# Kernel tuning notes

Measured on AMD Instinct MI355X. Metric: run time of the kernel, lower is better.

## Reference

```python
import jax, jax.numpy as jnp
import numpy as np

M1, M2 = 16, 16  # Fourier modes per dim


def conv1x1(x, w, b):
    # x: [B,Ci,H,W], w: [Co,Ci], b: [Co]
    return jnp.einsum('bihw,oi->bohw', x, w) + b[None, :, None, None]


def fno_block(x, wr, wi, bw, bb):
    # x: [B,C,H,W]; wr/wi: [C,C,M1,M2]; bw: [C,C]; bb: [C]
    H, W = x.shape[-2], x.shape[-1]
    x_fft = jnp.fft.rfftn(x, axes=(-2, -1), norm='ortho')[:, :, :M1, :M2]
    w = (wr + 1j * wi).astype(jnp.complex64)
    out_fft = jnp.einsum('bikl,iokl->bokl', x_fft, w)
    # irfftn with s zero-pads truncated modes back to full spatial size
    x_spec = jnp.fft.irfftn(out_fft, s=(H, W), axes=(-2, -1), norm='ortho')
    return jax.nn.gelu(x_spec + conv1x1(x, bw, bb), approximate=False)


def setup_inputs() -> dict:
    key = jax.random.key(0)
    ks = jax.random.split(key, 8)
    B, in_c, H, W = 4, 3, 256, 256
    out_c, n_blocks, width = 4, 4, 32
    scale = 1.0 / (width * width)
    return {
        'x': jax.random.normal(ks[0], (B, in_c, H, W), jnp.float32),
        'lift_w': jax.random.normal(ks[1], (width, in_c), jnp.float32) * 0.1,
        'lift_b': jnp.zeros((width,), jnp.float32),
        'wr': jax.random.normal(ks[2], (out_c, n_blocks, width, width, M1, M2), jnp.float32) * scale,
        'wi': jax.random.normal(ks[3], (out_c, n_blocks, width, width, M1, M2), jnp.float32) * scale,
        'byp_w': jax.random.normal(ks[4], (out_c, n_blocks, width, width), jnp.float32) * 0.1,
        'byp_b': jnp.zeros((out_c, n_blocks, width), jnp.float32),
        'proj_w': jax.random.normal(ks[5], (1, width), jnp.float32) * 0.1,
        'proj_b': jnp.zeros((1,), jnp.float32),
    }


def reference(x, lift_w, lift_b, wr, wi, byp_w, byp_b, proj_w, proj_b):
    out_c, n_blocks = wr.shape[0], wr.shape[1]
    x0 = conv1x1(x, lift_w, lift_b)
    outputs = []
    for o in range(out_c):
        xb = x0
        for n in range(n_blocks):
            xb = fno_block(xb, wr[o, n], wi[o, n], byp_w[o, n], byp_b[o, n])
        outputs.append(conv1x1(xb, proj_w, proj_b))
    return jnp.concatenate(outputs, axis=1)
```

## Files before the change

kernel.cpp:

```cpp
#include <hip/hip_runtime.h>

#define NB 4
#define NC 32
#define NH 256
#define NW 256
#define NM 16
constexpr int NPIX = NH * NW;
constexpr int NP = NB * NC * NPIX;
constexpr int ZG = NB * NC * NM * NM * 2;

typedef short bf16x8 __attribute__((ext_vector_type(8)));
typedef float f32x4  __attribute__((ext_vector_type(4)));
typedef unsigned short u16;
typedef unsigned int u32;

#define MFMA16(a, b, c) __builtin_amdgcn_mfma_f32_16x16x32_bf16(a, b, c, 0, 0, 0)

__device__ __forceinline__ u16 f2bf(float f) {
    unsigned u = __float_as_uint(f);
    u += 0x7FFFu + ((u >> 16) & 1u);
    return (u16)(u >> 16);
}
__device__ __forceinline__ float bf2f(u16 h) {
    return __uint_as_float(((unsigned)h) << 16);
}
__device__ __forceinline__ u32 packsplit(float f) {
    const u16 hi = f2bf(f);
    const u16 lo = f2bf(f - bf2f(hi));
    return (u32)hi | ((u32)lo << 16);
}

__device__ __forceinline__ float gelu_fast(float v) {
    const float ax = fabsf(v) * 0.70710678118654752f;
    const float t = __builtin_amdgcn_rcpf(1.0f + 0.3275911f * ax);
    const float y = t * (0.254829592f + t * (-0.284496736f + t * (1.421413741f +
                    t * (-1.453152027f + t * 1.061405429f))));
    const float e = __expf(-ax * ax);
    float er = 1.0f - y * e;
    er = copysignf(er, v);
    return 0.5f * v * (1.0f + er);
}

__global__ __launch_bounds__(256) void tab_prep(
    u16* __restrict__ cwhi, u16* __restrict__ cwlo,
    u16* __restrict__ ebhi, u16* __restrict__ eblo)
{
    const int id = blockIdx.x * 256 + threadIdx.x;
    if (id < 8192) {
        const int nn = id >> 5, k = id & 31;
        const int m = ((k & 15) * nn) & 255;
        float s, c;
        sincospif((float)m * (2.0f / 256.0f), &s, &c);
        const float v = (k < 16) ? c : s;
        const u16 hi = f2bf(v);
        cwhi[id] = hi;
        cwlo[id] = f2bf(v - bf2f(hi));
    } else {
        const int id2 = id - 8192;
        const int row = id2 >> 8, w = id2 & 255;
        const int m = ((row & 15) * w) & 255;
        float s, c;
        sincospif((float)m * (2.0f / 256.0f), &s, &c);
        const float v = 0.0625f * ((row < 16) ? c : s);
        const u16 hi = f2bf(v);
        ebhi[id2] = hi;
        eblo[id2] = f2bf(v - bf2f(hi));
    }
}

__global__ __launch_bounds__(256) void s1_lift(
    const float* __restrict__ src,
    const float* __restrict__ lift_w,
    const float* __restrict__ lift_b,
    const u16* __restrict__ ebhi,
    const u16* __restrict__ eblo,
    u32* __restrict__ ypk)
{
    __shared__ u32 TrPk[64][33];

    const int tid = threadIdx.x;
    const int c  = blockIdx.x;
    const int b  = blockIdx.y;
    const int hq = blockIdx.z;
    const int wv = tid >> 6, lane = tid & 63;
    const int mrow = lane & 15, q = lane >> 4;
    const int hbase = hq * 64 + wv * 16;

    const float lw0 = lift_w[c * 3 + 0], lw1 = lift_w[c * 3 + 1], lw2 = lift_w[c * 3 + 2];
    const float lb = lift_b[c];
    const float* sb = src + (size_t)b * 3 * NPIX;

    f32x4 acc[2] = {};
    for (int ks = 0; ks < 8; ++ks) {
        bf16x8 bh[2], bl[2];
        #pragma unroll
        for (int nt = 0; nt < 2; ++nt) {
            const int off = (nt * 16 + mrow) * 256 + ks * 32 + q * 8;
            bh[nt] = *(const bf16x8*)(ebhi + off);
            bl[nt] = *(const bf16x8*)(eblo + off);
        }
        const float* xp = sb + (size_t)(hbase + mrow) * NW + ks * 32 + q * 8;
        const float4 p0a = *(const float4*)(xp);
        const float4 p0b = *(const float4*)(xp + 4);
        const float4 p1a = *(const float4*)(xp + NPIX);
        const float4 p1b = *(const float4*)(xp + NPIX + 4);
        const float4 p2a = *(const float4*)(xp + 2 * NPIX);
        const float4 p2b = *(const float4*)(xp + 2 * NPIX + 4);
        float v[8];
        v[0] = lw0 * p0a.x + lw1 * p1a.x + lw2 * p2a.x + lb;
        v[1] = lw0 * p0a.y + lw1 * p1a.y + lw2 * p2a.y + lb;
        v[2] = lw0 * p0a.z + lw1 * p1a.z + lw2 * p2a.z + lb;
        v[3] = lw0 * p0a.w + lw1 * p1a.w + lw2 * p2a.w + lb;
        v[4] = lw0 * p0b.x + lw1 * p1b.x + lw2 * p2b.x + lb;
        v[5] = lw0 * p0b.y + lw1 * p1b.y + lw2 * p2b.y + lb;
        v[6] = lw0 * p0b.z + lw1 * p1b.z + lw2 * p2b.z + lb;
        v[7] = lw0 * p0b.w + lw1 * p1b.w + lw2 * p2b.w + lb;
        bf16x8 xh, xl;
        #pragma unroll
        for (int j = 0; j < 8; ++j) {
            const u16 hi = f2bf(v[j]);
            xh[j] = (short)hi;
            xl[j] = (short)f2bf(v[j] - bf2f(hi));
        }
        #pragma unroll
        for (int nt = 0; nt < 2; ++nt) {
            acc[nt] = MFMA16(xh, bh[nt], acc[nt]);
            acc[nt] = MFMA16(xh, bl[nt], acc[nt]);
            acc[nt] = MFMA16(xl, bh[nt], acc[nt]);
        }
    }

    #pragma unroll
    for (int nt = 0; nt < 2; ++nt) {
        #pragma unroll
        for (int r = 0; r < 4; ++r)
            TrPk[wv * 16 + q * 4 + r][nt * 16 + mrow] = packsplit(acc[nt][r]);
    }
    __syncthreads();

    #pragma unroll
    for (int i = 0; i < 8; ++i) {
        const int idx = i * 256 + tid;
        const int hl = idx >> 5, combo = idx & 31;
        ypk[((size_t)b * 256 + hq * 64 + hl) * 1024 + c * 32 + combo] = TrPk[hl][combo];
    }
}

__global__ __launch_bounds__(256) void s2_kernel(
    const u32* __restrict__ ypk,
    const u16* __restrict__ ebhi,
    const u16* __restrict__ eblo,
    float* __restrict__ zred)
{
    __shared__ u32 Yl[256][33];
    __shared__ float P[32][33];

    const int tid = threadIdx.x;
    const int c  = blockIdx.x;
    const int gb = blockIdx.y;
    const int wv = tid >> 6, lane = tid & 63;
    const int mrow = lane & 15, q = lane >> 4;

    #pragma unroll
    for (int i = 0; i < 32; ++i) {
        const int idx = i * 256 + tid;
        const int h = idx >> 5, combo = idx & 31;
        Yl[h][combo] = ypk[((size_t)gb * 256 + h) * 1024 + c * 32 + combo];
    }
    __syncthreads();

    const int mt2 = wv >> 1, nt2 = wv & 1;
    const int wc = nt2 * 16 + mrow;
    f32x4 p = {};
    for (int ks = 0; ks < 8; ++ks) {
        const int aoff = (mt2 * 16 + mrow) * 256 + ks * 32 + q * 8;
        const bf16x8 ah = *(const bf16x8*)(ebhi + aoff);
        const bf16x8 al = *(const bf16x8*)(eblo + aoff);
        bf16x8 yh, yl;
        #pragma unroll
        for (int j = 0; j < 8; ++j) {
            const u32 v = Yl[ks * 32 + q * 8 + j][wc];
            yh[j] = (short)(v & 0xFFFFu);
            yl[j] = (short)(v >> 16);
        }
        p = MFMA16(ah, yh, p);
        p = MFMA16(ah, yl, p);
        p = MFMA16(al, yh, p);
    }
    #pragma unroll
    for (int r = 0; r < 4; ++r)
        P[mt2 * 16 + q * 4 + r][wc] = p[r];
    __syncthreads();

    const int k = tid >> 4, l = tid & 15;
    const float zr = P[k][l] - P[16 + k][16 + l];
    const float zi = -(P[k][16 + l] + P[16 + k][l]);
    const int idx = (gb * NC + c) * 256 + tid;
    zred[idx * 2 + 0] = zr;
    zred[idx * 2 + 1] = zi;
}

__global__ __launch_bounds__(256) void mix_kernel(
    const float* __restrict__ zred,
    float* __restrict__ zmix,
    const float* __restrict__ wr,
    const float* __restrict__ wi,
    int o0, int n, int zgmul)
{
    __shared__ float ps[4][NB][64][2];
    const int tid = threadIdx.x;
    const int oc = blockIdx.x, mq = blockIdx.y, g = blockIdx.z;
    const int o = o0 + g, zg = zgmul * g;
    const int ichunk = tid >> 6, ml = tid & 63;
    const int mode = mq * 64 + ml;

    const float* wrb = wr + (size_t)(o * 4 + n) * NC * NC * 256;
    const float* wib = wi + (size_t)(o * 4 + n) * NC * NC * 256;

    float orr[NB] = {0.f, 0.f, 0.f, 0.f};
    float oii[NB] = {0.f, 0.f, 0.f, 0.f};

    #pragma unroll
    for (int ii = 0; ii < 8; ++ii) {
        const int i = ichunk * 8 + ii;
        const float wrv = wrb[(i * NC + oc) * 256 + mode];
        const float wiv = wib[(i * NC + oc) * 256 + mode];
        #pragma unroll
        for (int b = 0; b < NB; ++b) {
            const float2 z = *(const float2*)&zred[(((zg * NB + b) * NC + i) * 256 + mode) * 2];
            orr[b] += z.x * wrv - z.y * wiv;
            oii[b] += z.x * wiv + z.y * wrv;
        }
    }
    #pragma unroll
    for (int b = 0; b < NB; ++b) {
        ps[ichunk][b][ml][0] = orr[b];
        ps[ichunk][b][ml][1] = oii[b];
    }
    __syncthreads();

    const int b2 = tid >> 6, ml2 = tid & 63;
    float re = 0.f, im = 0.f;
    #pragma unroll
    for (int ic = 0; ic < 4; ++ic) {
        re += ps[ic][b2][ml2][0];
        im += ps[ic][b2][ml2][1];
    }
    const int oidx = ((g * NB + b2) * NC + oc) * 256 + mq * 64 + ml2;
    zmix[oidx * 2 + 0] = re;
    zmix[oidx * 2 + 1] = im;
}

template<bool LIFT, bool FINAL, bool PRODY>
__global__ __launch_bounds__(256) void inv_kernel(
    const float* __restrict__ zmix,
    const void* __restrict__ srcv,
    const float* __restrict__ byp_w,
    const float* __restrict__ byp_b,
    const float* __restrict__ lift_w,
    const float* __restrict__ lift_b,
    const float* __restrict__ proj_w,
    const float* __restrict__ proj_b,
    const u16* __restrict__ cwhi,
    const u16* __restrict__ cwlo,
    const u16* __restrict__ ebhi,
    const u16* __restrict__ eblo,
    u32* __restrict__ ypk,
    void* __restrict__ dstv,
    int o0, int n)
{
    __shared__ float2 tw[256];
    __shared__ u16 Thi[NC * 40], Tlo[NC * 40];
    __shared__ u16 Whi[NC * 40], Wlo[NC * 40];
    __shared__ float bbl[NC];
    __shared__ float bweffs[NC * 3];
    __shared__ u16 Ghi[PRODY ? 32 * 264 : 1];
    __shared__ u16 Glo[PRODY ? 32 * 264 : 1];
    __shared__ u32 Ypks[PRODY ? 1024 : 1];

    const int tid = threadIdx.x;
    const int h = blockIdx.x;
    const int gb = blockIdx.y;
    const int g = gb >> 2, b = gb & 3;
    const int o = o0 + g;

    {
        float s, cs;
        sincospif((float)tid * (2.0f / 256.0f), &s, &cs);
        tw[tid] = make_float2(cs, s);
    }

    const float* bwp = byp_w + (size_t)(o * 4 + n) * NC * NC;
    const float* bbp = byp_b + (o * 4 + n) * NC;

    if (LIFT) {
        if (tid < 96) {
            const int oc = tid / 3, j = tid % 3;
            float s = 0.f;
            for (int ic = 0; ic < NC; ++ic) s += bwp[oc * NC + ic] * lift_w[ic * 3 + j];
            bweffs[oc * 3 + j] = s;
        } else if (tid < 128) {
            const int oc = tid - 96;
            float s = bbp[oc];
            for (int ic = 0; ic < NC; ++ic) s += bwp[oc * NC + ic] * lift_b[ic];
            bbl[oc] = s;
        }
    } else {
        if (tid < NC) bbl[tid] = bbp[tid];
    }
    __syncthreads();

    for (int idx = tid; idx < NC * NC; idx += 256) {
        const int c = idx >> 5, ic = idx & 31;
        float v;
        if (LIFT) v = (ic < 3) ? bweffs[c * 3 + ic] : 0.f;
        else      v = bwp[idx];
        const u16 hi = f2bf(v);
        Whi[c * 40 + ic] = hi;
        Wlo[c * 40 + ic] = f2bf(v - bf2f(hi));
    }

    #pragma unroll
    for (int rep = 0; rep < 2; ++rep) {
        const int it = rep * 256 + tid;
        const int c = it >> 4, l = it & 15;
        const float sl = (l == 0 ? 1.0f : 2.0f) / 256.0f;
        const float* zp = zmix + ((size_t)(gb * NC + c) * 256 + l) * 2;
        float tr = 0.f, ti = 0.f;
        int m = 0;
        #pragma unroll
        for (int k = 0; k < NM; ++k) {
            const float2 z = *(const float2*)(zp + k * 32);
            const float2 t = tw[m];
            tr += z.x * t.x - z.y * t.y;
            ti += z.x * t.y + z.y * t.x;
            m = (m + h) & 255;
        }
        tr *= sl; ti *= sl;
        if (l == 0) tr += bbl[c];
        const u16 rh = f2bf(tr);
        Thi[c * 40 + l] = rh;
        Tlo[c * 40 + l] = f2bf(tr - bf2f(rh));
        const float nti_ = -ti;
        const u16 ih = f2bf(nti_);
        Thi[c * 40 + 16 + l] = ih;
        Tlo[c * 40 + 16 + l] = f2bf(nti_ - bf2f(ih));
    }
    __syncthreads();

    const int lane = tid & 63, wv = tid >> 6;
    const int mrow = lane & 15, q = lane >> 4;

    bf16x8 aThi[2], aTlo[2], aWhi[2], aWlo[2];
    #pragma unroll
    for (int mt = 0; mt < 2; ++mt) {
        const int ro = (mt * 16 + mrow) * 40 + 8 * q;
        aThi[mt] = *(const bf16x8*)&Thi[ro];
        aTlo[mt] = *(const bf16x8*)&Tlo[ro];
        aWhi[mt] = *(const bf16x8*)&Whi[ro];
        aWlo[mt] = *(const bf16x8*)&Wlo[ro];
    }

    float pwv[8];
    float pb = 0.f;
    if (FINAL) {
        #pragma unroll
        for (int mt = 0; mt < 2; ++mt)
            #pragma unroll
            for (int i = 0; i < 4; ++i)
                pwv[mt * 4 + i] = proj_w[mt * 16 + q * 4 + i];
        pb = proj_b[0];
    }

    const float* xbf = LIFT ? (const float*)srcv + (size_t)b * 3 * NPIX + h * NW : nullptr;
    const u32*   xbp = LIFT ? nullptr : (const u32*)srcv + (size_t)gb * NC * NPIX + h * NW;
    u32*   dstp = (u32*)dstv;
    float* dstf = (float*)dstv;

    for (int nti = 0; nti < 4; ++nti) {
        const int nt = wv * 4 + nti;
        const int ncol = nt * 16 + mrow;

        const bf16x8 cwh = *(const bf16x8*)(cwhi + ncol * 32 + 8 * q);
        const bf16x8 cwl = *(const bf16x8*)(cwlo + ncol * 32 + 8 * q);

        bf16x8 xh, xl;
        #pragma unroll
        for (int j = 0; j < 8; ++j) {
            const int k = 8 * q + j;
            if (LIFT) {
                const float v = (k < 3) ? xbf[(size_t)k * NPIX + ncol] : 0.f;
                const u16 hi = f2bf(v);
                xh[j] = (short)hi;
                xl[j] = (short)f2bf(v - bf2f(hi));
            } else {
                const u32 p = xbp[(size_t)k * NPIX + ncol];
                xh[j] = (short)(p & 0xFFFFu);
                xl[j] = (short)(p >> 16);
            }
        }

        float fpart = 0.f;
        #pragma unroll
        for (int mt = 0; mt < 2; ++mt) {
            f32x4 acc = {0.f, 0.f, 0.f, 0.f};
            acc = MFMA16(aThi[mt], cwh, acc);
            acc = MFMA16(aThi[mt], cwl, acc);
            acc = MFMA16(aTlo[mt], cwh, acc);
            acc = MFMA16(aWhi[mt], xh, acc);
            acc = MFMA16(aWhi[mt], xl, acc);
            acc = MFMA16(aWlo[mt], xh, acc);
            if (FINAL) {
                #pragma unroll
                for (int i = 0; i < 4; ++i)
                    fpart += gelu_fast(acc[i]) * pwv[mt * 4 + i];
            } else {
                #pragma unroll
                for (int i = 0; i < 4; ++i) {
                    const int c = mt * 16 + q * 4 + i;
                    const float gl = gelu_fast(acc[i]);
                    dstp[((size_t)gb * NC + c) * NPIX + h * NW + ncol] = packsplit(gl);
                    if (PRODY) {
                        const u16 hi = f2bf(gl);
                        Ghi[c * 264 + ncol] = hi;
                        Glo[c * 264 + ncol] = f2bf(gl - bf2f(hi));
                    }
                }
            }
        }
        if (FINAL) {
            fpart += __shfl_xor(fpart, 16);
            fpart += __shfl_xor(fpart, 32);
            if (q == 0) {
                dstf[(((size_t)b * 4 + o) * NH + h) * NW + nt * 16 + mrow] = fpart + pb;
            }
        }
    }

    if (PRODY) {
        __syncthreads();
        const int mt1 = wv >> 1, nt1 = wv & 1;
        f32x4 yacc = {};
        for (int ks = 0; ks < 8; ++ks) {
            const int ao = (mt1 * 16 + mrow) * 264 + ks * 32 + q * 8;
            const bf16x8 gh = *(const bf16x8*)&Ghi[ao];
            const bf16x8 gl = *(const bf16x8*)&Glo[ao];
            const int bo = (nt1 * 16 + mrow) * 256 + ks * 32 + q * 8;
            const bf16x8 bh = *(const bf16x8*)(ebhi + bo);
            const bf16x8 bl = *(const bf16x8*)(eblo + bo);
            yacc = MFMA16(gh, bh, yacc);
            yacc = MFMA16(gh, bl, yacc);
            yacc = MFMA16(gl, bh, yacc);
        }
        #pragma unroll
        for (int r = 0; r < 4; ++r) {
            const int c = mt1 * 16 + q * 4 + r;
            const int combo = nt1 * 16 + mrow;
            Ypks[c * 32 + combo] = packsplit(yacc[r]);
        }
        __syncthreads();
        u32* yout = ypk + ((size_t)gb * 256 + h) * 1024;
        #pragma unroll
        for (int i = 0; i < 4; ++i)
            yout[i * 256 + tid] = Ypks[i * 256 + tid];
    }
}

extern "C" void kernel_launch(void* const* d_in, const int* in_sizes, int n_in,
                              void* d_out, int out_size, void* d_ws, size_t ws_size,
                              hipStream_t stream)
{
    const float* x      = (const float*)d_in[0];
    const float* lift_w = (const float*)d_in[1];
    const float* lift_b = (const float*)d_in[2];
    const float* wr     = (const float*)d_in[3];
    const float* wi     = (const float*)d_in[4];
    const float* byp_w  = (const float*)d_in[5];
    const float* byp_b  = (const float*)d_in[6];
    const float* proj_w = (const float*)d_in[7];
    const float* proj_b = (const float*)d_in[8];
    float* ws  = (float*)d_ws;

    const int G = 2;

    u16* cwhi = (u16*)ws;
    u16* cwlo = cwhi + 8192;
    u16* ebhi = cwlo + 8192;
    u16* eblo = ebhi + 8192;
    float* zlift = ws + 16384;
    u32* ylift = (u32*)(zlift + 65536);
    u32* y     = ylift + (size_t)4 * 256 * 1024;
    float* zred = (float*)(y + (size_t)G * NB * 256 * 1024);
    float* zmix = zred + (size_t)G * ZG;
    u32* bufA = (u32*)(zmix + (size_t)G * ZG);
    u32* bufB = bufA + (size_t)G * NP;

    tab_prep<<<64, 256, 0, stream>>>(cwhi, cwlo, ebhi, eblo);

    s1_lift<<<dim3(NC, NB, 4), 256, 0, stream>>>(x, lift_w, lift_b, ebhi, eblo, ylift);
    s2_kernel<<<dim3(NC, NB), 256, 0, stream>>>(ylift, ebhi, eblo, zlift);

    for (int o0 = 0; o0 < 4; o0 += G) {
        const u32* rd = nullptr;
        u32* wrbuf = bufA;
        for (int n = 0; n < 4; ++n) {
            const bool lift = (n == 0);
            const bool fin  = (n == 3);

            if (!lift)
                s2_kernel<<<dim3(NC, G * NB), 256, 0, stream>>>(y, ebhi, eblo, zred);

            mix_kernel<<<dim3(NC, 4, G), 256, 0, stream>>>(
                lift ? zlift : zred, zmix, wr, wi, o0, n, lift ? 0 : 1);

            dim3 igrid(NH, G * NB);
            if (fin) {
                inv_kernel<false, true, false><<<igrid, 256, 0, stream>>>(
                    zmix, rd, byp_w, byp_b, lift_w, lift_b, proj_w, proj_b,
                    cwhi, cwlo, ebhi, eblo, y, d_out, o0, n);
            } else if (lift) {
                inv_kernel<true, false, true><<<igrid, 256, 0, stream>>>(
                    zmix, x, byp_w, byp_b, lift_w, lift_b, proj_w, proj_b,
                    cwhi, cwlo, ebhi, eblo, y, wrbuf, o0, n);
            } else {
                inv_kernel<false, false, true><<<igrid, 256, 0, stream>>>(
                    zmix, rd, byp_w, byp_b, lift_w, lift_b, proj_w, proj_b,
                    cwhi, cwlo, ebhi, eblo, y, wrbuf, o0, n);
            }
            rd = wrbuf;
            wrbuf = (wrbuf == bufA) ? bufB : bufA;
        }
    }
}
```

Before: 506.5 us.

## Shrink LDS with XOR swizzles, alias buffers, prefetch inputs early in inv_kernel

Replaces the padded LDS layouts (stride 40/264) with unpadded XOR-swizzled layouts and aliases the twiddle/bias scratch onto the G buffer. This cuts shared memory per block so more blocks fit per CU, and launch bounds now request 4 blocks per CU. It also issues the global input loads at kernel entry so their latency overlaps the twiddle and spectral setup, and drops the Ypks staging buffer and its barrier by writing Y straight to global. The costs are higher register pressure from the 32 prefetched values per thread and less coalesced Y stores.

```diff
diff --git a/kernel.cpp b/kernel.cpp
--- a/kernel.cpp
+++ b/kernel.cpp
@@ -252,7 +252,7 @@
 }
 
 template<bool LIFT, bool FINAL, bool PRODY>
-__global__ __launch_bounds__(256) void inv_kernel(
+__global__ __launch_bounds__(256, 4) void inv_kernel(
     const float* __restrict__ zmix,
     const void* __restrict__ srcv,
     const float* __restrict__ byp_w,
@@ -269,20 +269,47 @@
     void* __restrict__ dstv,
     int o0, int n)
 {
-    __shared__ float2 tw[256];
-    __shared__ u16 Thi[NC * 40], Tlo[NC * 40];
-    __shared__ u16 Whi[NC * 40], Wlo[NC * 40];
-    __shared__ float bbl[NC];
-    __shared__ float bweffs[NC * 3];
-    __shared__ u16 Ghi[PRODY ? 32 * 264 : 1];
-    __shared__ u16 Glo[PRODY ? 32 * 264 : 1];
-    __shared__ u32 Ypks[PRODY ? 1024 : 1];
+    __shared__ __align__(16) u16 Thi[NC * 32], Tlo[NC * 32];
+    __shared__ __align__(16) u16 Whi[NC * 32], Wlo[NC * 32];
+    __shared__ __align__(16) u16 Ghi[PRODY ? NC * 256 : 1280];
+    __shared__ __align__(16) u16 Glo[PRODY ? NC * 256 : 8];
+
+    float2* const tw     = (float2*)Ghi;
+    float*  const bbl    = (float*)(Ghi + 1024);
+    float*  const bweffs = (float*)(Ghi + 1088);
 
     const int tid = threadIdx.x;
     const int h = blockIdx.x;
     const int gb = blockIdx.y;
     const int g = gb >> 2, b = gb & 3;
     const int o = o0 + g;
+    const int lane = tid & 63, wv = tid >> 6;
+    const int mrow = lane & 15, q = lane >> 4;
+
+    const float* xbf = LIFT ? (const float*)srcv + (size_t)b * 3 * NPIX + h * NW : nullptr;
+    const u32*   xbp = LIFT ? nullptr : (const u32*)srcv + (size_t)gb * NC * NPIX + h * NW;
+    u32*   dstp = (u32*)dstv;
+    float* dstf = (float*)dstv;
+
+    u32 xpre[4][8];
+    float xfpre[4][3];
+    if (!LIFT) {
+        #pragma unroll
+        for (int nti = 0; nti < 4; ++nti) {
+            const int ncol = (wv * 4 + nti) * 16 + mrow;
+            #pragma unroll
+            for (int j = 0; j < 8; ++j)
+                xpre[nti][j] = xbp[(size_t)(8 * q + j) * NPIX + ncol];
+        }
+    } else if (q == 0) {
+        #pragma unroll
+        for (int nti = 0; nti < 4; ++nti) {
+            const int ncol = (wv * 4 + nti) * 16 + mrow;
+            #pragma unroll
+            for (int j = 0; j < 3; ++j)
+                xfpre[nti][j] = xbf[(size_t)j * NPIX + ncol];
+        }
+    }
 
     {
         float s, cs;
@@ -316,8 +343,9 @@
         if (LIFT) v = (ic < 3) ? bweffs[c * 3 + ic] : 0.f;
         else      v = bwp[idx];
         const u16 hi = f2bf(v);
-        Whi[c * 40 + ic] = hi;
-        Wlo[c * 40 + ic] = f2bf(v - bf2f(hi));
+        const int widx = c * 32 + (ic ^ ((c & 3) << 3));
+        Whi[widx] = hi;
+        Wlo[widx] = f2bf(v - bf2f(hi));
     }
 
     #pragma unroll
@@ -338,23 +366,21 @@
         }
         tr *= sl; ti *= sl;
         if (l == 0) tr += bbl[c];
+        const int sw = (c & 3) << 3;
         const u16 rh = f2bf(tr);
-        Thi[c * 40 + l] = rh;
-        Tlo[c * 40 + l] = f2bf(tr - bf2f(rh));
+        Thi[c * 32 + (l ^ sw)] = rh;
+        Tlo[c * 32 + (l ^ sw)] = f2bf(tr - bf2f(rh));
         const float nti_ = -ti;
         const u16 ih = f2bf(nti_);
-        Thi[c * 40 + 16 + l] = ih;
-        Tlo[c * 40 + 16 + l] = f2bf(nti_ - bf2f(ih));
+        Thi[c * 32 + ((16 + l) ^ sw)] = ih;
+        Tlo[c * 32 + ((16 + l) ^ sw)] = f2bf(nti_ - bf2f(ih));
     }
     __syncthreads();
 
-    const int lane = tid & 63, wv = tid >> 6;
-    const int mrow = lane & 15, q = lane >> 4;
-
     bf16x8 aThi[2], aTlo[2], aWhi[2], aWlo[2];
     #pragma unroll
     for (int mt = 0; mt < 2; ++mt) {
-        const int ro = (mt * 16 + mrow) * 40 + 8 * q;
+        const int ro = (mt * 16 + mrow) * 32 + 8 * (q ^ (mrow & 3));
         aThi[mt] = *(const bf16x8*)&Thi[ro];
         aTlo[mt] = *(const bf16x8*)&Tlo[ro];
         aWhi[mt] = *(const bf16x8*)&Whi[ro];
@@ -372,11 +398,6 @@
         pb = proj_b[0];
     }
 
-    const float* xbf = LIFT ? (const float*)srcv + (size_t)b * 3 * NPIX + h * NW : nullptr;
-    const u32*   xbp = LIFT ? nullptr : (const u32*)srcv + (size_t)gb * NC * NPIX + h * NW;
-    u32*   dstp = (u32*)dstv;
-    float* dstf = (float*)dstv;
-
     for (int nti = 0; nti < 4; ++nti) {
         const int nt = wv * 4 + nti;
         const int ncol = nt * 16 + mrow;
@@ -387,14 +408,13 @@
         bf16x8 xh, xl;
         #pragma unroll
         for (int j = 0; j < 8; ++j) {
-            const int k = 8 * q + j;
             if (LIFT) {
-                const float v = (k < 3) ? xbf[(size_t)k * NPIX + ncol] : 0.f;
+                const float v = (q == 0 && j < 3) ? xfpre[nti][j] : 0.f;
                 const u16 hi = f2bf(v);
                 xh[j] = (short)hi;
                 xl[j] = (short)f2bf(v - bf2f(hi));
             } else {
-                const u32 p = xbp[(size_t)k * NPIX + ncol];
+                const u32 p = xpre[nti][j];
                 xh[j] = (short)(p & 0xFFFFu);
                 xl[j] = (short)(p >> 16);
             }
@@ -421,9 +441,10 @@
                     const float gl = gelu_fast(acc[i]);
                     dstp[((size_t)gb * NC + c) * NPIX + h * NW + ncol] = packsplit(gl);
                     if (PRODY) {
+                        const int gidx = c * 256 + (ncol ^ ((c & 7) << 3));
                         const u16 hi = f2bf(gl);
-                        Ghi[c * 264 + ncol] = hi;
-                        Glo[c * 264 + ncol] = f2bf(gl - bf2f(hi));
+                        Ghi[gidx] = hi;
+                        Glo[gidx] = f2bf(gl - bf2f(hi));
                     }
                 }
             }
@@ -442,7 +463,8 @@
         const int mt1 = wv >> 1, nt1 = wv & 1;
         f32x4 yacc = {};
         for (int ks = 0; ks < 8; ++ks) {
-            const int ao = (mt1 * 16 + mrow) * 264 + ks * 32 + q * 8;
+            const int r1 = mt1 * 16 + mrow;
+            const int ao = r1 * 256 + ((ks * 32 + q * 8) ^ ((r1 & 7) << 3));
             const bf16x8 gh = *(const bf16x8*)&Ghi[ao];
             const bf16x8 gl = *(const bf16x8*)&Glo[ao];
             const int bo = (nt1 * 16 + mrow) * 256 + ks * 32 + q * 8;
@@ -452,17 +474,13 @@
             yacc = MFMA16(gh, bl, yacc);
             yacc = MFMA16(gl, bh, yacc);
         }
+        u32* yout = ypk + ((size_t)gb * 256 + h) * 1024;
         #pragma unroll
         for (int r = 0; r < 4; ++r) {
             const int c = mt1 * 16 + q * 4 + r;
             const int combo = nt1 * 16 + mrow;
-            Ypks[c * 32 + combo] = packsplit(yacc[r]);
-        }
-        __syncthreads();
-        u32* yout = ypk + ((size_t)gb * 256 + h) * 1024;
-        #pragma unroll
-        for (int i = 0; i < 4; ++i)
-            yout[i * 256 + tid] = Ypks[i * 256 + tid];
+            yout[c * 32 + combo] = packsplit(yacc[r]);
+        }
     }
 }
 
```

Result: slower. 531.5 us (+4.9%).
